# Kernel optimization log

Measured on AMD Instinct MI355X. Metric: run time of the kernel, lower is better.

## Reference

```python
import jax, jax.numpy as jnp
import numpy as np
from jax import lax

B, CIN, COUT, H, W = 16, 32, 64, 64, 64
EPS = 1e-5
N_STEPS = 5  # dopri5 integrated 0->1; fixed step h=0.2 == original max_step

# Dormand-Prince (dopri5) tableau
A21 = 1/5
A31, A32 = 3/40, 9/40
A41, A42, A43 = 44/45, -56/15, 32/9
A51, A52, A53, A54 = 19372/6561, -25360/2187, 64448/6561, -212/729
A61, A62, A63, A64, A65 = 9017/3168, -355/33, 46732/5247, 49/176, -5103/18656
B1, B3, B4, B5, B6 = 35/384, 500/1113, 125/192, -2187/6784, 11/84


def conv2d(x, w, b=None, pad=1):
    y = lax.conv_general_dilated(x, w, (1, 1), [(pad, pad), (pad, pad)],
                                 dimension_numbers=('NCHW', 'OIHW', 'NCHW'))
    if b is not None:
        y = y + b.reshape(1, -1, 1, 1)
    return y


def batchnorm(x, gamma, beta):
    # training-mode BN: batch statistics over (N, H, W)
    m = jnp.mean(x, axis=(0, 2, 3), keepdims=True)
    v = jnp.var(x, axis=(0, 2, 3), keepdims=True)
    return (x - m) * lax.rsqrt(v + EPS) * gamma.reshape(1, -1, 1, 1) + beta.reshape(1, -1, 1, 1)


def ode_integrate(x0, w_ode, tg_w, tg_b):
    # dx/dt = gelu(x @ W) * 1/(1 + sigmoid(x @ tg_w.T + tg_b)); matmul over last (width) axis
    def f(x):
        tf = 1.0 / (1.0 + jax.nn.sigmoid(x @ tg_w.T + tg_b))
        return jax.nn.gelu(x @ w_ode, approximate=False) * tf

    h = 1.0 / N_STEPS

    def step(x, _):
        k1 = f(x)
        k2 = f(x + h * (A21 * k1))
        k3 = f(x + h * (A31 * k1 + A32 * k2))
        k4 = f(x + h * (A41 * k1 + A42 * k2 + A43 * k3))
        k5 = f(x + h * (A51 * k1 + A52 * k2 + A53 * k3 + A54 * k4))
        k6 = f(x + h * (A61 * k1 + A62 * k2 + A63 * k3 + A64 * k4 + A65 * k5))
        xn = x + h * (B1 * k1 + B3 * k3 + B4 * k4 + B5 * k5 + B6 * k6)
        return xn, None

    x1, _ = lax.scan(step, x0, None, length=N_STEPS)
    return x1


@jax.custom_vjp
def spike(x):
    return (x > 0).astype(x.dtype)

def _spike_fwd(x):
    return spike(x), x

def _spike_bwd(x, g):
    grad = 0.2 * jax.nn.relu(1.0 - jnp.abs(x / 2.0))
    return (grad * g,)

spike.defvjp(_spike_fwd, _spike_bwd)


def lif(x, w_ode, tg_w, tg_b, threshold):
    # mem_potential is None at first call -> zeros, so new_potential = ode_out
    ode_out = ode_integrate(x, w_ode, tg_w, tg_b)
    return spike(ode_out - threshold)


def setup_inputs() -> dict:
    key = jax.random.key(0)
    ks = jax.random.split(key, 12)
    s = lambda *sh: 1.0 / np.sqrt(np.prod(sh[1:]))
    d = {
        'x': jax.random.normal(ks[0], (B, CIN, H, W), jnp.float32),
        'conv1_w': jax.random.normal(ks[1], (COUT, CIN, 3, 3), jnp.float32) * 0.05,
        'conv1_b': jnp.zeros((COUT,), jnp.float32),
        'bn1_g': jnp.ones((COUT,), jnp.float32),
        'bn1_b': jnp.zeros((COUT,), jnp.float32),
        'ode1_w': jax.random.normal(ks[2], (COUT, COUT), jnp.float32) * 0.1,
        'tg1_w': jax.random.normal(ks[3], (COUT, COUT), jnp.float32) * (1.0 / np.sqrt(COUT)),
        'tg1_b': jnp.zeros((COUT,), jnp.float32),
        'conv2_w': jax.random.normal(ks[4], (COUT, COUT, 3, 3), jnp.float32) * 0.04,
        'bn2_g': jnp.ones((COUT,), jnp.float32),
        'bn2_b': jnp.zeros((COUT,), jnp.float32),
        'ode2_w': jax.random.normal(ks[5], (COUT, COUT), jnp.float32) * 0.1,
        'tg2_w': jax.random.normal(ks[6], (COUT, COUT), jnp.float32) * (1.0 / np.sqrt(COUT)),
        'tg2_b': jnp.zeros((COUT,), jnp.float32),
        'sc_w': jax.random.normal(ks[7], (COUT, CIN, 1, 1), jnp.float32) * 0.1,
        'sc_g': jnp.ones((COUT,), jnp.float32),
        'sc_b': jnp.zeros((COUT,), jnp.float32),
    }
    return d


def reference(x, conv1_w, conv1_b, bn1_g, bn1_b, ode1_w, tg1_w, tg1_b,
              conv2_w, bn2_g, bn2_b, ode2_w, tg2_w, tg2_b, sc_w, sc_g, sc_b):
    residual = batchnorm(conv2d(x, sc_w, None, pad=0), sc_g, sc_b)
    h1 = lif(batchnorm(conv2d(x, conv1_w, conv1_b), bn1_g, bn1_b), ode1_w, tg1_w, tg1_b, 0.3)
    h2 = lif(batchnorm(conv2d(h1, conv2_w, None), bn2_g, bn2_b), ode2_w, tg2_w, tg2_b, 0.5)
    return h2 + residual
```

## Files before the change

### kernel.cpp

```cpp
#include <hip/hip_runtime.h>
#include <math.h>


#define NELEM (16 * 64 * 64 * 64)

__device__ float  g_y1f[NELEM];
__device__ float  g_yscf[NELEM];
__device__ float  g_y2f[NELEM];
__device__ double g_part[384][1024];
__device__ double g_stats[384];
__device__ double g_prm[384];

__device__ __forceinline__ double wave_sum64(double v) {
#pragma unroll
  for (int m = 1; m < 64; m <<= 1) v += __shfl_xor(v, m);
  return v;
}

__global__ __launch_bounds__(256) void conv1_sc_kernel(
    const float* __restrict__ x, const float* __restrict__ w1,
    const float* __restrict__ b1, const float* __restrict__ scw)
{
  const int b = blockIdx.x >> 6, h = blockIdx.x & 63;
  const int w = threadIdx.x & 63;
  const int cog = __builtin_amdgcn_readfirstlane(threadIdx.x >> 6);
  __shared__ float xs[3][32][64];
  for (int i = threadIdx.x; i < 3 * 32 * 64; i += 256) {
    int kh = i >> 11, ci = (i >> 6) & 31, ww = i & 63;
    int hh = h + kh - 1;
    xs[kh][ci][ww] = ((unsigned)hh < 64u) ? x[((b * 32 + ci) << 12) + (hh << 6) + ww] : 0.f;
  }
  __syncthreads();

  float acc[16], asc[16];
#pragma unroll
  for (int i = 0; i < 16; ++i) { acc[i] = b1[cog * 16 + i]; asc[i] = 0.f; }

  for (int ci = 0; ci < 32; ++ci) {
    float xv[3][3];
#pragma unroll
    for (int kh = 0; kh < 3; ++kh) {
      xv[kh][0] = (w > 0)  ? xs[kh][ci][w - 1] : 0.f;
      xv[kh][1] = xs[kh][ci][w];
      xv[kh][2] = (w < 63) ? xs[kh][ci][w + 1] : 0.f;
    }
#pragma unroll
    for (int i = 0; i < 16; ++i) {
      const int co = cog * 16 + i;
      const float* wp = &w1[(co * 32 + ci) * 9];
      float a = acc[i];
#pragma unroll
      for (int k = 0; k < 9; ++k) a = fmaf(xv[k / 3][k % 3], wp[k], a);
      acc[i] = a;
      asc[i] = fmaf(xv[1][1], scw[co * 32 + ci], asc[i]);
    }
  }

#pragma unroll
  for (int i = 0; i < 16; ++i) {
    const int co = cog * 16 + i;
    const int oidx = ((b * 64 + co) << 12) + (h << 6) + w;
    float v = acc[i], u = asc[i];
    g_y1f[oidx] = v;
    g_yscf[oidx] = u;
    double dv = (double)v, du = (double)u;
    double s = wave_sum64(dv), q = wave_sum64(dv * dv);
    double ss = wave_sum64(du), qq = wave_sum64(du * du);
    if (w == 0) {
      g_part[co][blockIdx.x] = s;        g_part[64 + co][blockIdx.x] = q;
      g_part[128 + co][blockIdx.x] = ss; g_part[192 + co][blockIdx.x] = qq;
    }
  }
}

__global__ __launch_bounds__(256) void conv2_kernel(const float* __restrict__ w2)
{
  const int b = blockIdx.x >> 6, h = blockIdx.x & 63;
  const int w = threadIdx.x & 63;
  const int cog = __builtin_amdgcn_readfirstlane(threadIdx.x >> 6);
  __shared__ float xs[3][64][64];
  for (int i = threadIdx.x; i < 3 * 64 * 64; i += 256) {
    int kh = i >> 12, ci = (i >> 6) & 63, ww = i & 63;
    int hh = h + kh - 1;
    xs[kh][ci][ww] = ((unsigned)hh < 64u) ? g_y1f[((b * 64 + ci) << 12) + (hh << 6) + ww] : 0.f;
  }
  __syncthreads();

  float acc[16];
#pragma unroll
  for (int i = 0; i < 16; ++i) acc[i] = 0.f;

  for (int ci = 0; ci < 64; ++ci) {
    float xv[3][3];
#pragma unroll
    for (int kh = 0; kh < 3; ++kh) {
      xv[kh][0] = (w > 0)  ? xs[kh][ci][w - 1] : 0.f;
      xv[kh][1] = xs[kh][ci][w];
      xv[kh][2] = (w < 63) ? xs[kh][ci][w + 1] : 0.f;
    }
#pragma unroll
    for (int i = 0; i < 16; ++i) {
      const int co = cog * 16 + i;
      const float* wp = &w2[(co * 64 + ci) * 9];
      float a = acc[i];
#pragma unroll
      for (int k = 0; k < 9; ++k) a = fmaf(xv[k / 3][k % 3], wp[k], a);
      acc[i] = a;
    }
  }

#pragma unroll
  for (int i = 0; i < 16; ++i) {
    const int co = cog * 16 + i;
    float v = acc[i];
    g_y2f[((b * 64 + co) << 12) + (h << 6) + w] = v;
    double dv = (double)v;
    double s = wave_sum64(dv), q = wave_sum64(dv * dv);
    if (w == 0) { g_part[256 + co][blockIdx.x] = s; g_part[320 + co][blockIdx.x] = q; }
  }
}

__global__ __launch_bounds__(256) void reduce_stats(int base)
{
  const int row = base + blockIdx.x;
  const int t = threadIdx.x;
  double s = g_part[row][t] + g_part[row][t + 256] + g_part[row][t + 512] + g_part[row][t + 768];
  s = wave_sum64(s);
  __shared__ double ls[4];
  if ((t & 63) == 0) ls[t >> 6] = s;
  __syncthreads();
  if (t == 0) g_stats[row] = ls[0] + ls[1] + ls[2] + ls[3];
}

__global__ void bn_params(int s_off, int q_off, int p_off,
                          const float* __restrict__ g, const float* __restrict__ bta)
{
  int c = threadIdx.x;
  const double inv = 1.0 / 65536.0;
  double m = g_stats[s_off + c] * inv;
  double v = g_stats[q_off + c] * inv - m * m;
  double rstd = 1.0 / sqrt(v + 1e-5);
  double sc = (double)g[c] * rstd;
  g_prm[p_off + c] = sc;
  g_prm[p_off + 64 + c] = (double)bta[c] - m * sc;
}

template <bool RES>
__global__ __launch_bounds__(256, 2) void ode_kernel(
    int prm_off, const float* __restrict__ wodep, const float* __restrict__ wtgp,
    const float* __restrict__ tgbp, float thr, float* __restrict__ outf)
{
  __shared__ float wosl[4096];
  __shared__ float wtsl[4096];
  __shared__ __align__(16) float xbuf[4][64];
  for (int t = threadIdx.x; t < 4096; t += 256) {
    wosl[t] = wodep[t];
    wtsl[t] = wtgp[(t & 63) * 64 + (t >> 6)];
  }
  __syncthreads();

  const int lane = threadIdx.x & 63;
  const int wv = __builtin_amdgcn_readfirstlane(threadIdx.x >> 6);
  float wo[64], wt[64];
#pragma unroll
  for (int i = 0; i < 64; ++i) wo[i] = wosl[(i << 6) + lane];
#pragma unroll
  for (int i = 0; i < 64; ++i) wt[i] = wtsl[(i << 6) + lane];
  const float tb = tgbp[lane];
  float* __restrict__ xrow = xbuf[wv];

  auto feval = [&](float xs) -> float {
    __builtin_amdgcn_sched_barrier(0);
    xrow[lane] = xs;
    float ao0 = 0.f, ao1 = 0.f, ao2 = 0.f, ao3 = 0.f;
    float at0 = 0.f, at1 = 0.f, at2 = 0.f, at3 = 0.f;
#pragma unroll
    for (int i = 0; i < 64; i += 4) {
      float4 xq = *reinterpret_cast<const float4*>(&xrow[i]);
      ao0 = fmaf(xq.x, wo[i + 0], ao0);  at0 = fmaf(xq.x, wt[i + 0], at0);
      ao1 = fmaf(xq.y, wo[i + 1], ao1);  at1 = fmaf(xq.y, wt[i + 1], at1);
      ao2 = fmaf(xq.z, wo[i + 2], ao2);  at2 = fmaf(xq.z, wt[i + 2], at2);
      ao3 = fmaf(xq.w, wo[i + 3], ao3);  at3 = fmaf(xq.w, wt[i + 3], at3);
    }
    float ao = (ao0 + ao1) + (ao2 + ao3);
    float z = ((at0 + at1) + (at2 + at3)) + tb;
    float g = 0.5f * ao * (1.f + erff(ao * 0.70710678118654752440f));
    float e = expf(-z);
    float tf = 1.f - 1.f / (2.f + e);
    return g * tf;
  };

  const float H = (float)(1.0 / 5.0);
  const float A21 = (float)(1.0 / 5.0);
  const float A31 = (float)(3.0 / 40.0), A32 = (float)(9.0 / 40.0);
  const float A41 = (float)(44.0 / 45.0), A42 = (float)(-56.0 / 15.0), A43 = (float)(32.0 / 9.0);
  const float A51 = (float)(19372.0 / 6561.0), A52 = (float)(-25360.0 / 2187.0),
              A53 = (float)(64448.0 / 6561.0), A54 = (float)(-212.0 / 729.0);
  const float A61 = (float)(9017.0 / 3168.0), A62 = (float)(-355.0 / 33.0),
              A63 = (float)(46732.0 / 5247.0), A64 = (float)(49.0 / 176.0),
              A65 = (float)(-5103.0 / 18656.0);
  const float B1 = (float)(35.0 / 384.0), B3 = (float)(500.0 / 1113.0),
              B4 = (float)(125.0 / 192.0), B5 = (float)(-2187.0 / 6784.0),
              B6 = (float)(11.0 / 84.0);

  const int base = blockIdx.x * 8 + wv * 2;
#pragma unroll 1
  for (int r = 0; r < 2; ++r) {
    const int row = base + r;
    const int c = (row >> 6) & 63;
    const int idx = (row << 6) + lane;
    const double psc = g_prm[prm_off + c], psh = g_prm[prm_off + 64 + c];
    const float yv = RES ? g_y2f[idx] : g_y1f[idx];
    float xv = (float)fma((double)yv, psc, psh);

#pragma unroll 1
    for (int st5 = 0; st5 < 5; ++st5) {
      float k1 = feval(xv);
      float k2 = feval(xv + H * (A21 * k1));
      float k3 = feval(xv + H * (A31 * k1 + A32 * k2));
      float k4 = feval(xv + H * (A41 * k1 + A42 * k2 + A43 * k3));
      float k5 = feval(xv + H * (A51 * k1 + A52 * k2 + A53 * k3 + A54 * k4));
      float k6 = feval(xv + H * (A61 * k1 + A62 * k2 + A63 * k3 + A64 * k4 + A65 * k5));
      xv = xv + H * (B1 * k1 + B3 * k3 + B4 * k4 + B5 * k5 + B6 * k6);
    }

    float o = (xv - thr > 0.f) ? 1.f : 0.f;
    if (RES) {
      double res = fma((double)g_yscf[idx], g_prm[128 + c], g_prm[192 + c]);
      outf[idx] = (float)((double)o + res);
    } else {
      g_y1f[idx] = o;
    }
  }
}

extern "C" void kernel_launch(void* const* d_in, const int* in_sizes, int n_in,
                              void* d_out, int out_size, void* d_ws, size_t ws_size,
                              hipStream_t stream)
{
  const float* x    = (const float*)d_in[0];
  const float* c1w  = (const float*)d_in[1];
  const float* c1b  = (const float*)d_in[2];
  const float* bn1g = (const float*)d_in[3];
  const float* bn1b = (const float*)d_in[4];
  const float* o1w  = (const float*)d_in[5];
  const float* t1w  = (const float*)d_in[6];
  const float* t1b  = (const float*)d_in[7];
  const float* c2w  = (const float*)d_in[8];
  const float* bn2g = (const float*)d_in[9];
  const float* bn2b = (const float*)d_in[10];
  const float* o2w  = (const float*)d_in[11];
  const float* t2w  = (const float*)d_in[12];
  const float* t2b  = (const float*)d_in[13];
  const float* scw  = (const float*)d_in[14];
  const float* scg  = (const float*)d_in[15];
  const float* scb  = (const float*)d_in[16];

  conv1_sc_kernel<<<1024, 256, 0, stream>>>(x, c1w, c1b, scw);
  reduce_stats<<<256, 256, 0, stream>>>(0);
  bn_params<<<1, 64, 0, stream>>>(0, 64, 0, bn1g, bn1b);
  bn_params<<<1, 64, 0, stream>>>(128, 192, 128, scg, scb);

  ode_kernel<false><<<8192, 256, 0, stream>>>(0, o1w, t1w, t1b, 0.3f, nullptr);

  conv2_kernel<<<1024, 256, 0, stream>>>(c2w);
  reduce_stats<<<128, 256, 0, stream>>>(256);
  bn_params<<<1, 64, 0, stream>>>(256, 320, 256, bn2g, bn2b);

  ode_kernel<true><<<8192, 256, 0, stream>>>(256, o2w, t2w, t2b, 0.5f, (float*)d_out);
}
```

Baseline: 1.764 ms.

## Batch four rows per wave in ODE kernel, read weights from LDS

```diff
diff --git a/kernel.cpp b/kernel.cpp
--- a/kernel.cpp
+++ b/kernel.cpp
@@ -146,13 +146,13 @@
 }
 
 template <bool RES>
-__global__ __launch_bounds__(256, 2) void ode_kernel(
+__global__ __launch_bounds__(256, 4) void ode_kernel(
     int prm_off, const float* __restrict__ wodep, const float* __restrict__ wtgp,
     const float* __restrict__ tgbp, float thr, float* __restrict__ outf)
 {
   __shared__ float wosl[4096];
   __shared__ float wtsl[4096];
-  __shared__ __align__(16) float xbuf[4][64];
+  __shared__ __align__(16) float xbuf[4][4][64];
   for (int t = threadIdx.x; t < 4096; t += 256) {
     wosl[t] = wodep[t];
     wtsl[t] = wtgp[(t & 63) * 64 + (t >> 6)];
@@ -161,33 +161,44 @@
 
   const int lane = threadIdx.x & 63;
   const int wv = __builtin_amdgcn_readfirstlane(threadIdx.x >> 6);
-  float wo[64], wt[64];
-#pragma unroll
-  for (int i = 0; i < 64; ++i) wo[i] = wosl[(i << 6) + lane];
-#pragma unroll
-  for (int i = 0; i < 64; ++i) wt[i] = wtsl[(i << 6) + lane];
   const float tb = tgbp[lane];
-  float* __restrict__ xrow = xbuf[wv];
-
-  auto feval = [&](float xs) -> float {
+  float* __restrict__ xrow = &xbuf[wv][0][0];
+
+  const int base = blockIdx.x * 16 + wv * 4;
+  const int c = (base >> 6) & 63;
+  const double psc = g_prm[prm_off + c], psh = g_prm[prm_off + 64 + c];
+
+  auto feval4 = [&](const float* xs, float* kout) {
     __builtin_amdgcn_sched_barrier(0);
-    xrow[lane] = xs;
-    float ao0 = 0.f, ao1 = 0.f, ao2 = 0.f, ao3 = 0.f;
-    float at0 = 0.f, at1 = 0.f, at2 = 0.f, at3 = 0.f;
-#pragma unroll
-    for (int i = 0; i < 64; i += 4) {
-      float4 xq = *reinterpret_cast<const float4*>(&xrow[i]);
-      ao0 = fmaf(xq.x, wo[i + 0], ao0);  at0 = fmaf(xq.x, wt[i + 0], at0);
-      ao1 = fmaf(xq.y, wo[i + 1], ao1);  at1 = fmaf(xq.y, wt[i + 1], at1);
-      ao2 = fmaf(xq.z, wo[i + 2], ao2);  at2 = fmaf(xq.z, wt[i + 2], at2);
-      ao3 = fmaf(xq.w, wo[i + 3], ao3);  at3 = fmaf(xq.w, wt[i + 3], at3);
-    }
-    float ao = (ao0 + ao1) + (ao2 + ao3);
-    float z = ((at0 + at1) + (at2 + at3)) + tb;
-    float g = 0.5f * ao * (1.f + erff(ao * 0.70710678118654752440f));
-    float e = expf(-z);
-    float tf = 1.f - 1.f / (2.f + e);
-    return g * tf;
+#pragma unroll
+    for (int r = 0; r < 4; ++r) xrow[r * 64 + lane] = xs[r];
+    float ao[4] = {0.f, 0.f, 0.f, 0.f};
+    float at4[4] = {0.f, 0.f, 0.f, 0.f};
+#pragma unroll 1
+    for (int q = 0; q < 16; ++q) {
+      float4 xq[4];
+#pragma unroll
+      for (int r = 0; r < 4; ++r)
+        xq[r] = *reinterpret_cast<const float4*>(&xrow[r * 64 + q * 4]);
+#pragma unroll
+      for (int u = 0; u < 4; ++u) {
+        const float wov = wosl[(q * 4 + u) * 64 + lane];
+        const float wtv = wtsl[(q * 4 + u) * 64 + lane];
+#pragma unroll
+        for (int r = 0; r < 4; ++r) {
+          const float xu = (&xq[r].x)[u];
+          ao[r]  = fmaf(xu, wov, ao[r]);
+          at4[r] = fmaf(xu, wtv, at4[r]);
+        }
+      }
+    }
+#pragma unroll
+    for (int r = 0; r < 4; ++r) {
+      float z = at4[r] + tb;
+      float g = 0.5f * ao[r] * (1.f + erff(ao[r] * 0.70710678118654752440f));
+      float e = expf(-z);
+      kout[r] = g * (1.f - 1.f / (2.f + e));
+    }
   };
 
   const float H = (float)(1.0 / 5.0);
@@ -203,28 +214,44 @@
               B4 = (float)(125.0 / 192.0), B5 = (float)(-2187.0 / 6784.0),
               B6 = (float)(11.0 / 84.0);
 
-  const int base = blockIdx.x * 8 + wv * 2;
+  float xv[4];
+#pragma unroll
+  for (int r = 0; r < 4; ++r) {
+    const int idx = ((base + r) << 6) + lane;
+    const float yv = RES ? g_y2f[idx] : g_y1f[idx];
+    xv[r] = (float)fma((double)yv, psc, psh);
+  }
+
 #pragma unroll 1
-  for (int r = 0; r < 2; ++r) {
-    const int row = base + r;
-    const int c = (row >> 6) & 63;
-    const int idx = (row << 6) + lane;
-    const double psc = g_prm[prm_off + c], psh = g_prm[prm_off + 64 + c];
-    const float yv = RES ? g_y2f[idx] : g_y1f[idx];
-    float xv = (float)fma((double)yv, psc, psh);
-
-#pragma unroll 1
-    for (int st5 = 0; st5 < 5; ++st5) {
-      float k1 = feval(xv);
-      float k2 = feval(xv + H * (A21 * k1));
-      float k3 = feval(xv + H * (A31 * k1 + A32 * k2));
-      float k4 = feval(xv + H * (A41 * k1 + A42 * k2 + A43 * k3));
-      float k5 = feval(xv + H * (A51 * k1 + A52 * k2 + A53 * k3 + A54 * k4));
-      float k6 = feval(xv + H * (A61 * k1 + A62 * k2 + A63 * k3 + A64 * k4 + A65 * k5));
-      xv = xv + H * (B1 * k1 + B3 * k3 + B4 * k4 + B5 * k5 + B6 * k6);
-    }
-
-    float o = (xv - thr > 0.f) ? 1.f : 0.f;
+  for (int st5 = 0; st5 < 5; ++st5) {
+    float k1[4], k2[4], k3[4], k4[4], k5[4], k6[4], tmp[4];
+    feval4(xv, k1);
+#pragma unroll
+    for (int r = 0; r < 4; ++r) tmp[r] = xv[r] + H * (A21 * k1[r]);
+    feval4(tmp, k2);
+#pragma unroll
+    for (int r = 0; r < 4; ++r) tmp[r] = xv[r] + H * (A31 * k1[r] + A32 * k2[r]);
+    feval4(tmp, k3);
+#pragma unroll
+    for (int r = 0; r < 4; ++r) tmp[r] = xv[r] + H * (A41 * k1[r] + A42 * k2[r] + A43 * k3[r]);
+    feval4(tmp, k4);
+#pragma unroll
+    for (int r = 0; r < 4; ++r)
+      tmp[r] = xv[r] + H * (A51 * k1[r] + A52 * k2[r] + A53 * k3[r] + A54 * k4[r]);
+    feval4(tmp, k5);
+#pragma unroll
+    for (int r = 0; r < 4; ++r)
+      tmp[r] = xv[r] + H * (A61 * k1[r] + A62 * k2[r] + A63 * k3[r] + A64 * k4[r] + A65 * k5[r]);
+    feval4(tmp, k6);
+#pragma unroll
+    for (int r = 0; r < 4; ++r)
+      xv[r] = xv[r] + H * (B1 * k1[r] + B3 * k3[r] + B4 * k4[r] + B5 * k5[r] + B6 * k6[r]);
+  }
+
+#pragma unroll
+  for (int r = 0; r < 4; ++r) {
+    const int idx = ((base + r) << 6) + lane;
+    float o = (xv[r] - thr > 0.f) ? 1.f : 0.f;
     if (RES) {
       double res = fma((double)g_yscf[idx], g_prm[128 + c], g_prm[192 + c]);
       outf[idx] = (float)((double)o + res);
@@ -261,11 +288,11 @@
   bn_params<<<1, 64, 0, stream>>>(0, 64, 0, bn1g, bn1b);
   bn_params<<<1, 64, 0, stream>>>(128, 192, 128, scg, scb);
 
-  ode_kernel<false><<<8192, 256, 0, stream>>>(0, o1w, t1w, t1b, 0.3f, nullptr);
+  ode_kernel<false><<<4096, 256, 0, stream>>>(0, o1w, t1w, t1b, 0.3f, nullptr);
 
   conv2_kernel<<<1024, 256, 0, stream>>>(c2w);
   reduce_stats<<<128, 256, 0, stream>>>(256);
   bn_params<<<1, 64, 0, stream>>>(256, 320, 256, bn2g, bn2b);
 
-  ode_kernel<true><<<8192, 256, 0, stream>>>(256, o2w, t2w, t2b, 0.5f, (float*)d_out);
-}
+  ode_kernel<true><<<4096, 256, 0, stream>>>(256, o2w, t2w, t2b, 0.5f, (float*)d_out);
+}
```

Measured after the change: 1.729 ms. 1.02x faster.
